# Kernel tuning notes

Hardware: AMD Instinct MI355X
Metric: run time of the kernel (lower is better)

The kernel has to match this reference:

```python
import jax, jax.numpy as jnp
import numpy as np

N = 8192
IN_F = 512
OUT_F = 64
NEG_SLOPE = 0.01  # nn.LeakyReLU default
MASK_VAL = -1e9


def setup_inputs() -> dict:
    key = jax.random.key(0)
    k_h, k_adj, k_W, k_a = jax.random.split(key, 4)
    h = jax.random.normal(k_h, (N, IN_F), dtype=jnp.float32)
    adjacency = jax.random.randint(k_adj, (N, N), 0, 2, dtype=jnp.int32)
    # xavier_uniform bounds
    bW = float(np.sqrt(6.0 / (IN_F + OUT_F)))
    ba = float(np.sqrt(6.0 / (2 * OUT_F + 1)))
    W = jax.random.uniform(k_W, (IN_F, OUT_F), minval=-bW, maxval=bW, dtype=jnp.float32)
    a = jax.random.uniform(k_a, (2 * OUT_F, 1), minval=-ba, maxval=ba, dtype=jnp.float32)
    return {"h": h, "adjacency": adjacency, "W": W, "a": a}


def reference(h, adjacency, W, a):
    WH = h @ W                                  # [N, out_f]
    wh1 = WH @ a[:OUT_F, :]                     # [N, 1]
    wh2 = WH @ a[OUT_F:, :]                     # [N, 1]
    e = jax.nn.leaky_relu(wh1 + wh2.T, negative_slope=NEG_SLOPE)  # [N, N]
    attnt = jnp.where(adjacency > 0, e, jnp.float32(MASK_VAL))
    attnt = jax.nn.softmax(attnt, axis=1)       # row-wise softmax
    hfirst = attnt @ WH                         # [N, out_f]
    return jax.nn.elu(hfirst)
```

## Files before the change

kernel.cpp:

```cpp
#include <hip/hip_runtime.h>
#include <hip/hip_bf16.h>

#define N 8192
#define IN_F 512
#define OUT_F 64
#define S_SPLIT 16
#define JT (N / S_SPLIT)
#define LOG2E 1.4426950408889634f

typedef __attribute__((ext_vector_type(8))) short short8;
typedef __attribute__((ext_vector_type(4))) float floatx4;
typedef __attribute__((ext_vector_type(4))) int intx4;
typedef unsigned long long ull;

__device__ inline short f2bf(float x) {
    __hip_bfloat16 b = __float2bfloat16(x);
    return __builtin_bit_cast(short, b);
}

__global__ void k_wt(const float* __restrict__ W, short* __restrict__ WT) {
    int idx = blockIdx.x * 256 + threadIdx.x;
    int k = idx >> 6, f = idx & 63;
    WT[f * IN_F + k] = f2bf(W[k * OUT_F + f]);
}

__global__ __launch_bounds__(64) void k_wh(const float* __restrict__ h,
                                           const short* __restrict__ WT,
                                           const float* __restrict__ a,
                                           short* __restrict__ WHbT,
                                           float* __restrict__ wh1s,
                                           float* __restrict__ wh2s) {
    __shared__ float tile[OUT_F][17];
    int lane = threadIdx.x;
    int n = lane & 15, q = lane >> 4;
    int i0 = blockIdx.x * 16;
    int rowA = i0 + n;
    const float* hp = h + (size_t)rowA * IN_F + q * 8;
    floatx4 acc[4] = {};
    for (int k0 = 0; k0 < IN_F; k0 += 32) {
        floatx4 h0 = *(const floatx4*)(hp + k0);
        floatx4 h1 = *(const floatx4*)(hp + k0 + 4);
        short8 af;
#pragma unroll
        for (int j = 0; j < 4; j++) { af[j] = f2bf(h0[j]); af[j + 4] = f2bf(h1[j]); }
#pragma unroll
        for (int b = 0; b < 4; b++) {
            short8 bf_ = *(const short8*)(WT + (b * 16 + n) * IN_F + k0 + q * 8);
            acc[b] = __builtin_amdgcn_mfma_f32_16x16x32_bf16(af, bf_, acc[b], 0, 0, 0);
        }
    }
#pragma unroll
    for (int b = 0; b < 4; b++)
#pragma unroll
        for (int r = 0; r < 4; r++)
            tile[b * 16 + n][q * 4 + r] = acc[b][r];
    float a1v[4], a2v[4];
#pragma unroll
    for (int b = 0; b < 4; b++) { a1v[b] = a[b * 16 + n]; a2v[b] = a[OUT_F + b * 16 + n]; }
#pragma unroll
    for (int r = 0; r < 4; r++) {
        float s1 = 0.f, s2 = 0.f;
#pragma unroll
        for (int b = 0; b < 4; b++) { s1 += acc[b][r] * a1v[b]; s2 += acc[b][r] * a2v[b]; }
#pragma unroll
        for (int m = 1; m <= 8; m <<= 1) {
            s1 += __shfl_xor(s1, m, 64);
            s2 += __shfl_xor(s2, m, 64);
        }
        if (n == 0) {
            wh1s[i0 + q * 4 + r] = s1 * LOG2E;
            wh2s[i0 + q * 4 + r] = s2 * LOG2E;
        }
    }
    __syncthreads();
    const float* tc = tile[lane];
    short8 s0, s1v;
#pragma unroll
    for (int k = 0; k < 8; k++) { s0[k] = f2bf(tc[k]); s1v[k] = f2bf(tc[k + 8]); }
    *(short8*)(WHbT + (size_t)lane * N + i0) = s0;
    *(short8*)(WHbT + (size_t)lane * N + i0 + 8) = s1v;
}

__global__ __launch_bounds__(256) void k_attn(const int* __restrict__ adj,
                                              const short* __restrict__ WHbT,
                                              const float* __restrict__ wh1s,
                                              const float* __restrict__ wh2s,
                                              float* __restrict__ num_part,
                                              float* __restrict__ den_part) {
    __shared__ unsigned ldsm[4 * 16 * 17];
    int tid = threadIdx.x;
    int w = tid >> 6;
    int lane = tid & 63;
    int n = lane & 15, q = lane >> 4;
    int split = blockIdx.y;
    int j0 = split * JT;
    int i0 = (blockIdx.x * 4 + w) * 16;
    unsigned* mym = ldsm + w * 16 * 17;

    for (int r = 0; r < 16; r++) {
        const int* p = adj + (size_t)(i0 + r) * N + j0 + lane;
        ull m0 = __ballot(p[0]   > 0);
        ull m1 = __ballot(p[64]  > 0);
        ull m2 = __ballot(p[128] > 0);
        ull m3 = __ballot(p[192] > 0);
        ull m4 = __ballot(p[256] > 0);
        ull m5 = __ballot(p[320] > 0);
        ull m6 = __ballot(p[384] > 0);
        ull m7 = __ballot(p[448] > 0);
        if (lane < 16) {
            ull s0 = (lane & 2) ? m1 : m0;
            ull s1 = (lane & 2) ? m3 : m2;
            ull s2 = (lane & 2) ? m5 : m4;
            ull s3 = (lane & 2) ? m7 : m6;
            ull t0 = (lane & 4) ? s1 : s0;
            ull t1 = (lane & 4) ? s3 : s2;
            ull u  = (lane & 8) ? t1 : t0;
            unsigned dw = (lane & 1) ? (unsigned)(u >> 32) : (unsigned)u;
            mym[r * 17 + lane] = dw;
        }
    }

    float wh1f = wh1s[i0 + n];
    floatx4 acc[4] = {};
    floatx4 accd = {};
    const short* bp0 = WHbT + (size_t)n * N + j0 + q * 8;
    const float* w2p = wh2s + j0 + q * 8;
    int qs = q * 8;
    short8 ones;
#pragma unroll
    for (int k = 0; k < 8; k++) ones[k] = (short)0x3F80;

    for (int s = 0; s < 16; s++) {
        short8 bfr[4];
#pragma unroll
        for (int b = 0; b < 4; b++)
            bfr[b] = *(const short8*)(bp0 + (size_t)b * 16 * N + s * 32);
        unsigned md = mym[n * 17 + s];
        floatx4 w20 = *(const floatx4*)(w2p + s * 32);
        floatx4 w21 = *(const floatx4*)(w2p + s * 32 + 4);

        short8 af;
#pragma unroll
        for (int jj = 0; jj < 8; jj++) {
            float x = wh1f + ((jj < 4) ? w20[jj] : w21[jj - 4]);
            float t = fmaxf(x, 0.01f * x);
            float e = __builtin_amdgcn_exp2f(t);
            af[jj] = f2bf(((md >> (qs + jj)) & 1u) ? e : 0.f);
        }
#pragma unroll
        for (int b = 0; b < 4; b++)
            acc[b] = __builtin_amdgcn_mfma_f32_16x16x32_bf16(af, bfr[b], acc[b], 0, 0, 0);
        accd = __builtin_amdgcn_mfma_f32_16x16x32_bf16(af, ones, accd, 0, 0, 0);
    }

    if (n == 0) {
#pragma unroll
        for (int r = 0; r < 4; r++)
            den_part[(size_t)split * N + i0 + q * 4 + r] = accd[r];
    }
    float* np_ = num_part + (size_t)split * N * OUT_F;
#pragma unroll
    for (int b = 0; b < 4; b++)
#pragma unroll
        for (int r = 0; r < 4; r++)
            np_[(size_t)(i0 + q * 4 + r) * OUT_F + b * 16 + n] = acc[b][r];
}

__global__ void k_final(const float* __restrict__ num_part,
                        const float* __restrict__ den_part,
                        float* __restrict__ out) {
    int idx = blockIdx.x * 256 + threadIdx.x;
    int row = idx >> 6;
    float s = 0.f, d = 0.f;
#pragma unroll
    for (int sp = 0; sp < S_SPLIT; sp++) {
        s += num_part[(size_t)sp * N * OUT_F + idx];
        d += den_part[sp * N + row];
    }
    float x = s / d;
    out[idx] = (x > 0.f) ? x : (__expf(x) - 1.f);
}

extern "C" void kernel_launch(void* const* d_in, const int* in_sizes, int n_in,
                              void* d_out, int out_size, void* d_ws, size_t ws_size,
                              hipStream_t stream) {
    const float* h = (const float*)d_in[0];
    const int* adj = (const int*)d_in[1];
    const float* W = (const float*)d_in[2];
    const float* a = (const float*)d_in[3];
    float* out = (float*)d_out;

    char* ws = (char*)d_ws;
    short* WHbT  = (short*)(ws);
    short* WT    = (short*)(ws + (size_t)(1 << 20));
    float* wh1s  = (float*)(ws + (size_t)(1 << 20) + (64 << 10));
    float* wh2s  = wh1s + N;
    float* num_p = (float*)(ws + (size_t)(16 << 20));
    float* den_p = (float*)(ws + (size_t)(48 << 20));

    k_wt<<<dim3(128), dim3(256), 0, stream>>>(W, WT);
    k_wh<<<dim3(N / 16), dim3(64), 0, stream>>>(h, WT, a, WHbT, wh1s, wh2s);
    k_attn<<<dim3(N / 64, S_SPLIT), dim3(256), 0, stream>>>(adj, WHbT, wh1s, wh2s,
                                                            num_p, den_p);
    k_final<<<dim3((N * OUT_F) / 256), dim3(256), 0, stream>>>(num_p, den_p, out);
}
```

Before: 443.4 us.

## Pre-pack adjacency bitmask and WH fragments; widen attention tile to 64 rows per wave

Moves adjacency-to-bitmask packing into a separate streaming kernel. Adds a kernel that reorders WH into MFMA-fragment order so each lane loads its B operand with one contiguous load. Each wave now processes 64 query rows (4 row fragments) instead of 16, so every WH fragment load is reused across four rows, and the next mask chunk is prefetched. The aim is to cut redundant B-operand traffic and make the dominant adjacency read fully coalesced. The cost is more accumulator registers (80 floats per lane), possibly lower occupancy, two extra launches and fewer blocks in k_attn.

```diff
diff --git a/kernel.cpp b/kernel.cpp
--- a/kernel.cpp
+++ b/kernel.cpp
@@ -16,6 +16,32 @@
 __device__ inline short f2bf(float x) {
     __hip_bfloat16 b = __float2bfloat16(x);
     return __builtin_bit_cast(short, b);
+}
+
+__global__ __launch_bounds__(256) void k_pack(const int* __restrict__ adj,
+                                              unsigned* __restrict__ mask) {
+    int wv = (blockIdx.x * 256 + threadIdx.x) >> 6;
+    int lane = threadIdx.x & 63;
+    const int* p = adj + (size_t)wv * 512 + lane;
+    ull m0 = __ballot(p[0]   > 0);
+    ull m1 = __ballot(p[64]  > 0);
+    ull m2 = __ballot(p[128] > 0);
+    ull m3 = __ballot(p[192] > 0);
+    ull m4 = __ballot(p[256] > 0);
+    ull m5 = __ballot(p[320] > 0);
+    ull m6 = __ballot(p[384] > 0);
+    ull m7 = __ballot(p[448] > 0);
+    if (lane < 16) {
+        ull s0 = (lane & 2) ? m1 : m0;
+        ull s1 = (lane & 2) ? m3 : m2;
+        ull s2 = (lane & 2) ? m5 : m4;
+        ull s3 = (lane & 2) ? m7 : m6;
+        ull t0 = (lane & 4) ? s1 : s0;
+        ull t1 = (lane & 4) ? s3 : s2;
+        ull u  = (lane & 8) ? t1 : t0;
+        unsigned dw = (lane & 1) ? (unsigned)(u >> 32) : (unsigned)u;
+        mask[wv * 16 + lane] = dw;
+    }
 }
 
 __global__ void k_wt(const float* __restrict__ W, short* __restrict__ WT) {
@@ -81,89 +107,100 @@
     *(short8*)(WHbT + (size_t)lane * N + i0 + 8) = s1v;
 }
 
-__global__ __launch_bounds__(256) void k_attn(const int* __restrict__ adj,
-                                              const short* __restrict__ WHbT,
+__global__ __launch_bounds__(256) void k_bp(const short* __restrict__ WHbT,
+                                            short* __restrict__ BP) {
+    int g = blockIdx.x;
+    int b = threadIdx.x >> 6;
+    int lane = threadIdx.x & 63;
+    int n = lane & 15, q = lane >> 4;
+    short8 v = *(const short8*)(WHbT + (size_t)(b * 16 + n) * N + g * 32 + q * 8);
+    *(short8*)(BP + ((size_t)(g * 4 + b) * 64 + lane) * 8) = v;
+}
+
+__global__ __launch_bounds__(256) void k_attn(const unsigned* __restrict__ maskb,
+                                              const short* __restrict__ BP,
                                               const float* __restrict__ wh1s,
                                               const float* __restrict__ wh2s,
                                               float* __restrict__ num_part,
                                               float* __restrict__ den_part) {
-    __shared__ unsigned ldsm[4 * 16 * 17];
     int tid = threadIdx.x;
     int w = tid >> 6;
     int lane = tid & 63;
-    int n = lane & 15, q = lane >> 4;
+    int n = lane & 15, q = lane >> 4, qs = q * 8;
     int split = blockIdx.y;
     int j0 = split * JT;
-    int i0 = (blockIdx.x * 4 + w) * 16;
-    unsigned* mym = ldsm + w * 16 * 17;
-
-    for (int r = 0; r < 16; r++) {
-        const int* p = adj + (size_t)(i0 + r) * N + j0 + lane;
-        ull m0 = __ballot(p[0]   > 0);
-        ull m1 = __ballot(p[64]  > 0);
-        ull m2 = __ballot(p[128] > 0);
-        ull m3 = __ballot(p[192] > 0);
-        ull m4 = __ballot(p[256] > 0);
-        ull m5 = __ballot(p[320] > 0);
-        ull m6 = __ballot(p[384] > 0);
-        ull m7 = __ballot(p[448] > 0);
-        if (lane < 16) {
-            ull s0 = (lane & 2) ? m1 : m0;
-            ull s1 = (lane & 2) ? m3 : m2;
-            ull s2 = (lane & 2) ? m5 : m4;
-            ull s3 = (lane & 2) ? m7 : m6;
-            ull t0 = (lane & 4) ? s1 : s0;
-            ull t1 = (lane & 4) ? s3 : s2;
-            ull u  = (lane & 8) ? t1 : t0;
-            unsigned dw = (lane & 1) ? (unsigned)(u >> 32) : (unsigned)u;
-            mym[r * 17 + lane] = dw;
-        }
-    }
-
-    float wh1f = wh1s[i0 + n];
-    floatx4 acc[4] = {};
-    floatx4 accd = {};
-    const short* bp0 = WHbT + (size_t)n * N + j0 + q * 8;
-    const float* w2p = wh2s + j0 + q * 8;
-    int qs = q * 8;
+    int i0 = blockIdx.x * 256 + w * 64;
+
+    float wh1f[4];
+#pragma unroll
+    for (int rf = 0; rf < 4; rf++) wh1f[rf] = wh1s[i0 + rf * 16 + n];
+
+    floatx4 acc[4][4] = {};
+    floatx4 accd[4] = {};
+    const float* w2p = wh2s + j0 + qs;
+    const short8* bp = (const short8*)BP + (size_t)split * 4096 + lane;
     short8 ones;
 #pragma unroll
     for (int k = 0; k < 8; k++) ones[k] = (short)0x3F80;
 
-    for (int s = 0; s < 16; s++) {
-        short8 bfr[4];
+    intx4 mcur[4], mnxt[4];
+#pragma unroll
+    for (int rf = 0; rf < 4; rf++)
+        mcur[rf] = *(const intx4*)(maskb + (size_t)(i0 + rf * 16 + n) * 256 + split * 16);
+
+    for (int g = 0; g < 4; g++) {
+        if (g < 3) {
+#pragma unroll
+            for (int rf = 0; rf < 4; rf++)
+                mnxt[rf] = *(const intx4*)(maskb + (size_t)(i0 + rf * 16 + n) * 256
+                                           + split * 16 + (g + 1) * 4);
+        }
+#pragma unroll
+        for (int d = 0; d < 4; d++) {
+            int s = g * 4 + d;
+            short8 bfr[4];
+#pragma unroll
+            for (int b = 0; b < 4; b++)
+                bfr[b] = bp[s * 256 + b * 64];
+            floatx4 w20 = *(const floatx4*)(w2p + s * 32);
+            floatx4 w21 = *(const floatx4*)(w2p + s * 32 + 4);
+#pragma unroll
+            for (int rf = 0; rf < 4; rf++) {
+                unsigned md = (unsigned)mcur[rf][d];
+                short8 af;
+#pragma unroll
+                for (int jj = 0; jj < 8; jj++) {
+                    float x = wh1f[rf] + ((jj < 4) ? w20[jj] : w21[jj - 4]);
+                    float t = fmaxf(x, 0.01f * x);
+                    float e = __builtin_amdgcn_exp2f(t);
+                    af[jj] = f2bf(((md >> (qs + jj)) & 1u) ? e : 0.f);
+                }
+#pragma unroll
+                for (int b = 0; b < 4; b++)
+                    acc[rf][b] = __builtin_amdgcn_mfma_f32_16x16x32_bf16(af, bfr[b], acc[rf][b], 0, 0, 0);
+                accd[rf] = __builtin_amdgcn_mfma_f32_16x16x32_bf16(af, ones, accd[rf], 0, 0, 0);
+            }
+        }
+#pragma unroll
+        for (int rf = 0; rf < 4; rf++) mcur[rf] = mnxt[rf];
+    }
+
+#pragma unroll
+    for (int rf = 0; rf < 4; rf++) {
+        if (n == 0) {
+#pragma unroll
+            for (int r = 0; r < 4; r++)
+                den_part[(size_t)split * N + i0 + rf * 16 + q * 4 + r] = accd[rf][r];
+        }
+    }
+    float* np_ = num_part + (size_t)split * N * OUT_F;
+#pragma unroll
+    for (int rf = 0; rf < 4; rf++)
 #pragma unroll
         for (int b = 0; b < 4; b++)
-            bfr[b] = *(const short8*)(bp0 + (size_t)b * 16 * N + s * 32);
-        unsigned md = mym[n * 17 + s];
-        floatx4 w20 = *(const floatx4*)(w2p + s * 32);
-        floatx4 w21 = *(const floatx4*)(w2p + s * 32 + 4);
-
-        short8 af;
-#pragma unroll
-        for (int jj = 0; jj < 8; jj++) {
-            float x = wh1f + ((jj < 4) ? w20[jj] : w21[jj - 4]);
-            float t = fmaxf(x, 0.01f * x);
-            float e = __builtin_amdgcn_exp2f(t);
-            af[jj] = f2bf(((md >> (qs + jj)) & 1u) ? e : 0.f);
-        }
-#pragma unroll
-        for (int b = 0; b < 4; b++)
-            acc[b] = __builtin_amdgcn_mfma_f32_16x16x32_bf16(af, bfr[b], acc[b], 0, 0, 0);
-        accd = __builtin_amdgcn_mfma_f32_16x16x32_bf16(af, ones, accd, 0, 0, 0);
-    }
-
-    if (n == 0) {
-#pragma unroll
-        for (int r = 0; r < 4; r++)
-            den_part[(size_t)split * N + i0 + q * 4 + r] = accd[r];
-    }
-    float* np_ = num_part + (size_t)split * N * OUT_F;
-#pragma unroll
-    for (int b = 0; b < 4; b++)
-#pragma unroll
-        for (int r = 0; r < 4; r++)
-            np_[(size_t)(i0 + q * 4 + r) * OUT_F + b * 16 + n] = acc[b][r];
+#pragma unroll
+            for (int r = 0; r < 4; r++)
+                np_[(size_t)(i0 + rf * 16 + q * 4 + r) * OUT_F + b * 16 + n] = acc[rf][b][r];
 }
 
 __global__ void k_final(const float* __restrict__ num_part,
@@ -191,16 +228,20 @@
     float* out = (float*)d_out;
 
     char* ws = (char*)d_ws;
-    short* WHbT  = (short*)(ws);
-    short* WT    = (short*)(ws + (size_t)(1 << 20));
-    float* wh1s  = (float*)(ws + (size_t)(1 << 20) + (64 << 10));
-    float* wh2s  = wh1s + N;
-    float* num_p = (float*)(ws + (size_t)(16 << 20));
-    float* den_p = (float*)(ws + (size_t)(48 << 20));
-
+    short* WHbT     = (short*)(ws);
+    short* WT       = (short*)(ws + (size_t)(1 << 20));
+    float* wh1s     = (float*)(ws + (size_t)(1 << 20) + (64 << 10));
+    float* wh2s     = wh1s + N;
+    unsigned* maskb = (unsigned*)(ws + (size_t)(2 << 20));
+    short* BP       = (short*)(ws + (size_t)(12 << 20));
+    float* num_p    = (float*)(ws + (size_t)(16 << 20));
+    float* den_p    = (float*)(ws + (size_t)(48 << 20));
+
+    k_pack<<<dim3((N / 32) * (N / 256) * 4), dim3(256), 0, stream>>>(adj, maskb);
     k_wt<<<dim3(128), dim3(256), 0, stream>>>(W, WT);
     k_wh<<<dim3(N / 16), dim3(64), 0, stream>>>(h, WT, a, WHbT, wh1s, wh2s);
-    k_attn<<<dim3(N / 64, S_SPLIT), dim3(256), 0, stream>>>(adj, WHbT, wh1s, wh2s,
-                                                            num_p, den_p);
+    k_bp<<<dim3(256), dim3(256), 0, stream>>>(WHbT, BP);
+    k_attn<<<dim3(N / 256, S_SPLIT), dim3(256), 0, stream>>>(maskb, BP, wh1s, wh2s,
+                                                             num_p, den_p);
     k_final<<<dim3((N * OUT_F) / 256), dim3(256), 0, stream>>>(num_p, den_p, out);
 }
```

Measured after the change: 412.8 us. -6.9%, faster.
